# Kernel optimization log

Hardware: AMD Instinct MI355X
Metric: run time of the kernel (lower is better)

## Reference

```python
import jax, jax.numpy as jnp
import numpy as np

N = 100000        # nodes
E = 3200000       # edges (avg degree 32)
F_IN = 128        # input_dim
H = 64            # hidden_dim


def setup_inputs() -> dict:
    key = jax.random.key(0)
    ks = jax.random.split(key, 8)
    x = jax.random.normal(ks[0], (N, F_IN), dtype=jnp.float32)
    edge_index = jax.random.randint(ks[1], (2, E), 0, N, dtype=jnp.int64)
    # Glorot-ish init for GCNConv weights, zero bias (PyG default)
    def glorot(k, fan_in, fan_out):
        s = jnp.sqrt(6.0 / (fan_in + fan_out))
        return jax.random.uniform(k, (fan_in, fan_out), jnp.float32, -s, s)
    return {
        "x": x,
        "edge_index": edge_index,
        "W1": glorot(ks[2], F_IN, H), "b1": jnp.zeros((H,), jnp.float32),
        "W2": glorot(ks[3], H, H),    "b2": jnp.zeros((H,), jnp.float32),
        "W3": glorot(ks[4], H, H),    "b3": jnp.zeros((H,), jnp.float32),
    }


def _gcn_prep(edge_index):
    # add self-loops, compute symmetric normalization D^-1/2 (A+I) D^-1/2
    loop = jnp.arange(N, dtype=edge_index.dtype)
    src = jnp.concatenate([edge_index[0], loop])  # message sources
    dst = jnp.concatenate([edge_index[1], loop])  # aggregation targets
    deg = jax.ops.segment_sum(jnp.ones_like(dst, dtype=jnp.float32), dst, num_segments=N)
    dis = jnp.where(deg > 0, jax.lax.rsqrt(jnp.maximum(deg, 1.0)), 0.0)
    norm = dis[src] * dis[dst]  # [E+N]
    return src, dst, norm


def _gcn_conv(x, W, b, src, dst, norm):
    h = x @ W                                  # [N, H]
    msg = h[src] * norm[:, None]               # gather + scale, [E+N, H]
    out = jax.ops.segment_sum(msg, dst, num_segments=N)
    return out + b


def reference(x, edge_index, W1, b1, W2, b2, W3, b3):
    # GAEEncoder forward (eval mode: dropout p=0.2 is identity)
    src, dst, norm = _gcn_prep(edge_index)
    x = jax.nn.relu(_gcn_conv(x, W1, b1, src, dst, norm))
    x = jax.nn.relu(_gcn_conv(x, W2, b2, src, dst, norm))
    return _gcn_conv(x, W3, b3, src, dst, norm)
```

## Files before the change

kernel.cpp:

```cpp
#include <hip/hip_runtime.h>
#include <cstdint>

#define HDIM 64
#define BKT 98
#define BSHIFT 10
#define BCAP 36864

__device__ __forceinline__ float bflo(unsigned u) { return __uint_as_float(u << 16); }
__device__ __forceinline__ float bfhi(unsigned u) { return __uint_as_float(u & 0xffff0000u); }
__device__ __forceinline__ unsigned f2bf(float x) {
    unsigned b = __float_as_uint(x);
    return (b + 0x7fffu + ((b >> 16) & 1u)) >> 16;
}

__global__ void k_detect(const unsigned* ei, int* flag, int* tails) {
    __shared__ int ok;
    int t = threadIdx.x;
    if (t == 0) ok = 1;
    if (t < BKT) tails[t] = 0;
    __syncthreads();
    if (t < 128 && ei[2 * t + 1] != 0u) ok = 0;
    __syncthreads();
    if (t == 0) *flag = ok;
}

__device__ __forceinline__ int edge_val(const void* ei, int is64, long long idx) {
    if (is64) return (int)((const long long*)ei)[idx];
    return ((const int*)ei)[idx];
}

__global__ __launch_bounds__(1024) void k_bucket(const void* ei, const int* flag,
                                                 int* tails, unsigned* packed, int E) {
    __shared__ int wcnt[16][BKT];
    __shared__ int wbase[16][BKT];
    int tid = threadIdx.x;
    int lane = tid & 63, wid = tid >> 6;
    for (int i = tid; i < 16 * BKT; i += 1024) ((int*)wcnt)[i] = 0;
    __syncthreads();
    int is64 = *flag;
    int e = blockIdx.x * 1024 + tid;
    int b = -1; unsigned val = 0;
    if (e < E) {
        int d = edge_val(ei, is64, (long long)E + e);
        int s = edge_val(ei, is64, (long long)e);
        b = d >> BSHIFT;
        val = ((unsigned)(d & 1023) << 17) | (unsigned)s;
    }
    unsigned long long m = ~0ull;
#pragma unroll
    for (int bit = 0; bit < 7; bit++) {
        unsigned long long bb = __ballot(((unsigned)b >> bit) & 1);
        m &= ((((unsigned)b >> bit) & 1) ? bb : ~bb);
    }
    unsigned long long below = (lane == 0) ? 0ull : ((~0ull) >> (64 - lane));
    int rank = __popcll(m & below);
    if (b >= 0 && rank == 0) wcnt[wid][b] = __popcll(m);
    __syncthreads();
    if (tid < BKT) {
        int tot = 0;
        int pw[16];
#pragma unroll
        for (int w = 0; w < 16; w++) { pw[w] = tot; tot += wcnt[w][tid]; }
        int gb = (tot > 0) ? atomicAdd(&tails[tid], tot) : 0;
#pragma unroll
        for (int w = 0; w < 16; w++) wbase[w][tid] = gb + pw[w];
    }
    __syncthreads();
    if (b >= 0) {
        int pos = wbase[wid][b] + rank;
        if (pos < BCAP) packed[(size_t)b * BCAP + pos] = val;
    }
}

__global__ void k_base(const int* tails, int* bucket_base, int* rowptr, int N_) {
    __shared__ int sm[128];
    int t = threadIdx.x;
    int v = (t < BKT) ? min(tails[t], BCAP) : 0;
    sm[t] = v;
    __syncthreads();
    for (int off = 1; off < 128; off <<= 1) {
        int u = (t >= off) ? sm[t - off] : 0;
        __syncthreads();
        sm[t] += u;
        __syncthreads();
    }
    if (t < BKT) bucket_base[t] = sm[t] - v;
    if (t == BKT) { bucket_base[BKT] = sm[BKT - 1]; rowptr[N_] = sm[BKT - 1]; }
}

__global__ __launch_bounds__(1024) void k_build(const unsigned* packed, const int* tails,
                                                const int* bucket_base, int* rowptr,
                                                float* dis, int* col, int N_) {
    __shared__ int cnt[1024];
    __shared__ int pfx[1024];
    __shared__ int fill[1024];
    int b = blockIdx.x, tid = threadIdx.x;
    int nb_ = tails[b]; if (nb_ > BCAP) nb_ = BCAP;
    const unsigned* pb = packed + (size_t)b * BCAP;
    cnt[tid] = 0; fill[tid] = 0;
    __syncthreads();
    for (int s = tid; s < nb_; s += 1024)
        atomicAdd(&cnt[pb[s] >> 17], 1);
    __syncthreads();
    int v = cnt[tid];
    pfx[tid] = v;
    __syncthreads();
    for (int off = 1; off < 1024; off <<= 1) {
        int t = (tid >= off) ? pfx[tid - off] : 0;
        __syncthreads();
        pfx[tid] += t;
        __syncthreads();
    }
    int excl = pfx[tid] - v;
    int rowbase = bucket_base[b];
    int node = (b << BSHIFT) + tid;
    if (node < N_) {
        rowptr[node] = rowbase + excl;
        dis[node] = rsqrtf((float)(v + 1));
    }
    cnt[tid] = rowbase + excl;
    __syncthreads();
    for (int s = tid; s < nb_; s += 1024) {
        unsigned vv = pb[s];
        int dl = vv >> 17;
        int pos = cnt[dl] + atomicAdd(&fill[dl], 1);
        col[pos] = (int)(vv & 131071u);
    }
}

template <int K>
__device__ __forceinline__ int wswz(int lane, int k4) {
    if (K == 128) return k4 ^ (lane & 31);
    return ((k4 ^ (lane & 15)) + ((lane >> 4) << 2)) & 15;
}

template <int K, bool IN_BF16>
__global__ __launch_bounds__(256) void k_gemm_scale(const void* __restrict__ inp,
                                                    const float* __restrict__ W,
                                                    const float* __restrict__ dis,
                                                    unsigned* __restrict__ g2, int n) {
    constexpr int ROWS = (K == 128) ? 32 : 64;
    __shared__ float wt[64 * K];
    __shared__ float xs[ROWS * K];
    __shared__ float dsh[ROWS];
    int tid = threadIdx.x;
    for (int i = tid; i < K * 64; i += 256) {
        int k = i >> 6, f = i & 63;
        int k4 = k >> 2, j = k & 3;
        wt[f * K + (wswz<K>(f, k4) << 2) + j] = W[i];
    }
    int row0 = blockIdx.x * ROWS;
    int nrow = min(ROWS, n - row0);
    if (IN_BF16) {
        const unsigned* src = (const unsigned*)inp + (size_t)row0 * (K / 2);
        int nw = nrow * (K / 2);
        for (int i = tid; i < nw; i += 256) {
            unsigned u = src[i];
            xs[2 * i] = bflo(u);
            xs[2 * i + 1] = bfhi(u);
        }
    } else {
        const float4* src4 = (const float4*)((const float*)inp + (size_t)row0 * K);
        int nf4 = nrow * (K / 4);
        float4* xs4 = (float4*)xs;
        for (int i = tid; i < nf4; i += 256) xs4[i] = src4[i];
    }
    if (tid < nrow) dsh[tid] = dis[row0 + tid];
    __syncthreads();
    int lane = tid & 63, wid = tid >> 6;
    const float* wtl = wt + lane * K;
    constexpr int RW = ROWS / 4;
    for (int q = 0; q < RW; q += 4) {
        int rq = wid * RW + q;
        const float* x0 = xs + (size_t)(rq + 0) * K;
        const float* x1 = xs + (size_t)(rq + 1) * K;
        const float* x2 = xs + (size_t)(rq + 2) * K;
        const float* x3 = xs + (size_t)(rq + 3) * K;
        float a0 = 0.f, a1 = 0.f, a2 = 0.f, a3 = 0.f;
#pragma unroll 4
        for (int k4 = 0; k4 < K / 4; k4++) {
            float4 wv = *(const float4*)(wtl + (wswz<K>(lane, k4) << 2));
            float4 v0 = *(const float4*)(x0 + k4 * 4);
            float4 v1 = *(const float4*)(x1 + k4 * 4);
            float4 v2 = *(const float4*)(x2 + k4 * 4);
            float4 v3 = *(const float4*)(x3 + k4 * 4);
            a0 = fmaf(v0.x, wv.x, a0); a0 = fmaf(v0.y, wv.y, a0);
            a0 = fmaf(v0.z, wv.z, a0); a0 = fmaf(v0.w, wv.w, a0);
            a1 = fmaf(v1.x, wv.x, a1); a1 = fmaf(v1.y, wv.y, a1);
            a1 = fmaf(v1.z, wv.z, a1); a1 = fmaf(v1.w, wv.w, a1);
            a2 = fmaf(v2.x, wv.x, a2); a2 = fmaf(v2.y, wv.y, a2);
            a2 = fmaf(v2.z, wv.z, a2); a2 = fmaf(v2.w, wv.w, a2);
            a3 = fmaf(v3.x, wv.x, a3); a3 = fmaf(v3.y, wv.y, a3);
            a3 = fmaf(v3.z, wv.z, a3); a3 = fmaf(v3.w, wv.w, a3);
        }
        int gr = row0 + rq;
        bool wr = ((lane & 1) == 0);
        int wi = lane >> 1;
#pragma unroll
        for (int i = 0; i < 4; i++) {
            float a = (i == 0) ? a0 : (i == 1) ? a1 : (i == 2) ? a2 : a3;
            float v = a * dsh[rq + i];
            float p = __shfl_xor(v, 1);
            if (wr && gr + i < n)
                g2[(size_t)(gr + i) * 32 + wi] = f2bf(v) | (f2bf(p) << 16);
        }
    }
}

template <bool RELU, bool OUT32>
__global__ __launch_bounds__(256) void k_aggregate(const unsigned* __restrict__ g2,
                                                   const int* __restrict__ rowptr,
                                                   const int* __restrict__ col,
                                                   const float* __restrict__ dis,
                                                   const float* __restrict__ bias,
                                                   void* __restrict__ outp, int n) {
    int lane = threadIdx.x & 63;
    int wid = threadIdx.x >> 6;
    int li = lane & 15;
    int q = lane >> 4;
    int node = blockIdx.x * 4 + wid;
    if (node >= n) return;
    const uint2* g2v = (const uint2*)g2;
    float s0 = 0.f, s1 = 0.f, s2 = 0.f, s3 = 0.f;
    if (q == 0) {
        uint2 u = g2v[(size_t)node * 16 + li];
        s0 = bflo(u.x); s1 = bfhi(u.x); s2 = bflo(u.y); s3 = bfhi(u.y);
    }
    int e = rowptr[node], end = rowptr[node + 1];
    for (; e + 31 < end; e += 32) {
        int c0 = col[e + q],      c1 = col[e + 4 + q],  c2 = col[e + 8 + q],  c3 = col[e + 12 + q];
        int c4 = col[e + 16 + q], c5 = col[e + 20 + q], c6 = col[e + 24 + q], c7 = col[e + 28 + q];
        uint2 u0 = g2v[(size_t)c0 * 16 + li];
        uint2 u1 = g2v[(size_t)c1 * 16 + li];
        uint2 u2 = g2v[(size_t)c2 * 16 + li];
        uint2 u3 = g2v[(size_t)c3 * 16 + li];
        uint2 u4 = g2v[(size_t)c4 * 16 + li];
        uint2 u5 = g2v[(size_t)c5 * 16 + li];
        uint2 u6 = g2v[(size_t)c6 * 16 + li];
        uint2 u7 = g2v[(size_t)c7 * 16 + li];
        s0 += ((bflo(u0.x) + bflo(u1.x)) + (bflo(u2.x) + bflo(u3.x)))
            + ((bflo(u4.x) + bflo(u5.x)) + (bflo(u6.x) + bflo(u7.x)));
        s1 += ((bfhi(u0.x) + bfhi(u1.x)) + (bfhi(u2.x) + bfhi(u3.x)))
            + ((bfhi(u4.x) + bfhi(u5.x)) + (bfhi(u6.x) + bfhi(u7.x)));
        s2 += ((bflo(u0.y) + bflo(u1.y)) + (bflo(u2.y) + bflo(u3.y)))
            + ((bflo(u4.y) + bflo(u5.y)) + (bflo(u6.y) + bflo(u7.y)));
        s3 += ((bfhi(u0.y) + bfhi(u1.y)) + (bfhi(u2.y) + bfhi(u3.y)))
            + ((bfhi(u4.y) + bfhi(u5.y)) + (bfhi(u6.y) + bfhi(u7.y)));
    }
    for (; e + 15 < end; e += 16) {
        int c0 = col[e + q], c1 = col[e + 4 + q], c2 = col[e + 8 + q], c3 = col[e + 12 + q];
        uint2 u0 = g2v[(size_t)c0 * 16 + li];
        uint2 u1 = g2v[(size_t)c1 * 16 + li];
        uint2 u2 = g2v[(size_t)c2 * 16 + li];
        uint2 u3 = g2v[(size_t)c3 * 16 + li];
        s0 += ((bflo(u0.x) + bflo(u1.x)) + (bflo(u2.x) + bflo(u3.x)));
        s1 += ((bfhi(u0.x) + bfhi(u1.x)) + (bfhi(u2.x) + bfhi(u3.x)));
        s2 += ((bflo(u0.y) + bflo(u1.y)) + (bflo(u2.y) + bflo(u3.y)));
        s3 += ((bfhi(u0.y) + bfhi(u1.y)) + (bfhi(u2.y) + bfhi(u3.y)));
    }
    for (; e + 3 < end; e += 4) {
        int c = col[e + q];
        uint2 u = g2v[(size_t)c * 16 + li];
        s0 += bflo(u.x); s1 += bfhi(u.x); s2 += bflo(u.y); s3 += bfhi(u.y);
    }
    if (e < end) {
        int idx = e + q;
        bool valid = idx < end;
        int c = valid ? col[idx] : col[end - 1];
        uint2 u = g2v[(size_t)c * 16 + li];
        if (valid) { s0 += bflo(u.x); s1 += bfhi(u.x); s2 += bflo(u.y); s3 += bfhi(u.y); }
    }
    s0 += __shfl_xor(s0, 32); s0 += __shfl_xor(s0, 16);
    s1 += __shfl_xor(s1, 32); s1 += __shfl_xor(s1, 16);
    s2 += __shfl_xor(s2, 32); s2 += __shfl_xor(s2, 16);
    s3 += __shfl_xor(s3, 32); s3 += __shfl_xor(s3, 16);
    float4 b4 = ((const float4*)bias)[li];
    float dn = dis[node];
    float o0 = fmaf(dn, s0, b4.x);
    float o1 = fmaf(dn, s1, b4.y);
    float o2 = fmaf(dn, s2, b4.z);
    float o3 = fmaf(dn, s3, b4.w);
    if (RELU) {
        o0 = fmaxf(o0, 0.f); o1 = fmaxf(o1, 0.f);
        o2 = fmaxf(o2, 0.f); o3 = fmaxf(o3, 0.f);
    }
    if (q == 0) {
        if (OUT32) {
            ((float4*)outp)[(size_t)node * 16 + li] = make_float4(o0, o1, o2, o3);
        } else {
            uint2 st;
            st.x = f2bf(o0) | (f2bf(o1) << 16);
            st.y = f2bf(o2) | (f2bf(o3) << 16);
            ((uint2*)outp)[(size_t)node * 16 + li] = st;
        }
    }
}

extern "C" void kernel_launch(void* const* d_in, const int* in_sizes, int n_in,
                              void* d_out, int out_size, void* d_ws, size_t ws_size,
                              hipStream_t stream) {
    const float* x  = (const float*)d_in[0];
    const void*  ei = d_in[1];
    const float* W1 = (const float*)d_in[2];
    const float* b1 = (const float*)d_in[3];
    const float* W2 = (const float*)d_in[4];
    const float* b2 = (const float*)d_in[5];
    const float* W3 = (const float*)d_in[6];
    const float* b3 = (const float*)d_in[7];

    const int N = in_sizes[0] / 128;
    const int E = in_sizes[1] / 2;

    char* ws = (char*)d_ws;
    auto alloc = [&](size_t bytes) {
        char* p = ws;
        ws += ((bytes + 255) / 256) * 256;
        return p;
    };
    int*   flag   = (int*)alloc(4);
    int*   tails  = (int*)alloc(BKT * 4);
    int*   bbase  = (int*)alloc((BKT + 1) * 4);
    int*   rowptr = (int*)alloc((size_t)(N + 1) * 4);
    float* dis    = (float*)alloc((size_t)N * 4);
    int*   col    = (int*)alloc((size_t)E * 4);
    unsigned* bufA = (unsigned*)alloc((size_t)N * HDIM * 4);
    unsigned* bufB = (unsigned*)alloc((size_t)N * HDIM * 4);
    unsigned* packed = bufA;

    k_detect<<<1, 128, 0, stream>>>((const unsigned*)ei, flag, tails);
    k_bucket<<<(E + 1023) / 1024, 1024, 0, stream>>>(ei, flag, tails, packed, E);
    k_base<<<1, 128, 0, stream>>>(tails, bbase, rowptr, N);
    k_build<<<BKT, 1024, 0, stream>>>(packed, tails, bbase, rowptr, dis, col, N);

    const int aggGrid = (N + 3) / 4;

    k_gemm_scale<128, false><<<(N + 31) / 32, 256, 0, stream>>>(x, W1, dis, bufA, N);
    k_aggregate<true, false><<<aggGrid, 256, 0, stream>>>(bufA, rowptr, col, dis, b1, bufB, N);
    k_gemm_scale<64, true><<<(N + 63) / 64, 256, 0, stream>>>(bufB, W2, dis, bufA, N);
    k_aggregate<true, false><<<aggGrid, 256, 0, stream>>>(bufA, rowptr, col, dis, b2, bufB, N);
    k_gemm_scale<64, true><<<(N + 63) / 64, 256, 0, stream>>>(bufB, W3, dis, bufA, N);
    k_aggregate<false, true><<<aggGrid, 256, 0, stream>>>(bufA, rowptr, col, dis, b3, d_out, N);
}
```

Baseline: 445.6 us.

## Fold detect and base-scan kernels into bucket/build and coarsen bucket blocks

Removes the separate dtype-detect and bucket-prefix-scan kernels. Each bucket block now detects int64 itself, and each build block recomputes the 98-entry bucket prefix scan redundantly. The zeroing of tails moves to a memset. Each bucket block now processes 4096 edges instead of 1024, cutting the number of global atomicAdds on the tails array by about four times. The cost is more shared memory per bucket block and redundant small scans in every build block.

Measured after the change: 414.0 us, median of 2. 1.08x faster.

```diff
diff --git a/kernel.cpp b/kernel.cpp
--- a/kernel.cpp
+++ b/kernel.cpp
@@ -5,6 +5,7 @@
 #define BKT 98
 #define BSHIFT 10
 #define BCAP 36864
+#define ECHUNK 4096
 
 __device__ __forceinline__ float bflo(unsigned u) { return __uint_as_float(u << 16); }
 __device__ __forceinline__ float bfhi(unsigned u) { return __uint_as_float(u & 0xffff0000u); }
@@ -13,89 +14,91 @@
     return (b + 0x7fffu + ((b >> 16) & 1u)) >> 16;
 }
 
-__global__ void k_detect(const unsigned* ei, int* flag, int* tails) {
-    __shared__ int ok;
-    int t = threadIdx.x;
-    if (t == 0) ok = 1;
-    if (t < BKT) tails[t] = 0;
-    __syncthreads();
-    if (t < 128 && ei[2 * t + 1] != 0u) ok = 0;
-    __syncthreads();
-    if (t == 0) *flag = ok;
-}
-
 __device__ __forceinline__ int edge_val(const void* ei, int is64, long long idx) {
     if (is64) return (int)((const long long*)ei)[idx];
     return ((const int*)ei)[idx];
 }
 
-__global__ __launch_bounds__(1024) void k_bucket(const void* ei, const int* flag,
-                                                 int* tails, unsigned* packed, int E) {
-    __shared__ int wcnt[16][BKT];
-    __shared__ int wbase[16][BKT];
+__global__ __launch_bounds__(1024) void k_bucket(const unsigned* ei32, int* tails,
+                                                 unsigned* packed, int E) {
+    __shared__ int wcnt[4][16][BKT];
+    __shared__ int wpre[4][16][BKT];
+    __shared__ int gbase[BKT];
+    __shared__ int is64_s;
     int tid = threadIdx.x;
     int lane = tid & 63, wid = tid >> 6;
-    for (int i = tid; i < 16 * BKT; i += 1024) ((int*)wcnt)[i] = 0;
-    __syncthreads();
-    int is64 = *flag;
-    int e = blockIdx.x * 1024 + tid;
-    int b = -1; unsigned val = 0;
-    if (e < E) {
-        int d = edge_val(ei, is64, (long long)E + e);
-        int s = edge_val(ei, is64, (long long)e);
-        b = d >> BSHIFT;
-        val = ((unsigned)(d & 1023) << 17) | (unsigned)s;
-    }
-    unsigned long long m = ~0ull;
-#pragma unroll
-    for (int bit = 0; bit < 7; bit++) {
-        unsigned long long bb = __ballot(((unsigned)b >> bit) & 1);
-        m &= ((((unsigned)b >> bit) & 1) ? bb : ~bb);
-    }
+    for (int i = tid; i < 4 * 16 * BKT; i += 1024) ((int*)wcnt)[i] = 0;
+    if (tid == 0) is64_s = 1;
+    __syncthreads();
+    if (tid < 128 && ei32[2 * tid + 1] != 0u) is64_s = 0;
+    __syncthreads();
+    int is64 = is64_s;
+    const void* ei = ei32;
+    int b[4]; unsigned val[4]; int rank[4];
+    int e0 = blockIdx.x * ECHUNK;
     unsigned long long below = (lane == 0) ? 0ull : ((~0ull) >> (64 - lane));
-    int rank = __popcll(m & below);
-    if (b >= 0 && rank == 0) wcnt[wid][b] = __popcll(m);
+#pragma unroll
+    for (int r = 0; r < 4; r++) {
+        int e = e0 + r * 1024 + tid;
+        b[r] = -1; val[r] = 0;
+        if (e < E) {
+            int d = edge_val(ei, is64, (long long)E + e);
+            int s = edge_val(ei, is64, (long long)e);
+            b[r] = d >> BSHIFT;
+            val[r] = ((unsigned)(d & 1023) << 17) | (unsigned)s;
+        }
+        unsigned long long m = ~0ull;
+#pragma unroll
+        for (int bit = 0; bit < 7; bit++) {
+            unsigned long long bb = __ballot(((unsigned)b[r] >> bit) & 1);
+            m &= ((((unsigned)b[r] >> bit) & 1) ? bb : ~bb);
+        }
+        rank[r] = __popcll(m & below);
+        if (b[r] >= 0 && rank[r] == 0) wcnt[r][wid][b[r]] = __popcll(m);
+    }
     __syncthreads();
     if (tid < BKT) {
         int tot = 0;
-        int pw[16];
-#pragma unroll
-        for (int w = 0; w < 16; w++) { pw[w] = tot; tot += wcnt[w][tid]; }
-        int gb = (tot > 0) ? atomicAdd(&tails[tid], tot) : 0;
-#pragma unroll
-        for (int w = 0; w < 16; w++) wbase[w][tid] = gb + pw[w];
-    }
-    __syncthreads();
-    if (b >= 0) {
-        int pos = wbase[wid][b] + rank;
-        if (pos < BCAP) packed[(size_t)b * BCAP + pos] = val;
-    }
-}
-
-__global__ void k_base(const int* tails, int* bucket_base, int* rowptr, int N_) {
-    __shared__ int sm[128];
-    int t = threadIdx.x;
-    int v = (t < BKT) ? min(tails[t], BCAP) : 0;
-    sm[t] = v;
-    __syncthreads();
-    for (int off = 1; off < 128; off <<= 1) {
-        int u = (t >= off) ? sm[t - off] : 0;
-        __syncthreads();
-        sm[t] += u;
-        __syncthreads();
-    }
-    if (t < BKT) bucket_base[t] = sm[t] - v;
-    if (t == BKT) { bucket_base[BKT] = sm[BKT - 1]; rowptr[N_] = sm[BKT - 1]; }
+#pragma unroll
+        for (int r = 0; r < 4; r++)
+#pragma unroll
+            for (int w = 0; w < 16; w++) {
+                wpre[r][w][tid] = tot;
+                tot += wcnt[r][w][tid];
+            }
+        gbase[tid] = (tot > 0) ? atomicAdd(&tails[tid], tot) : 0;
+    }
+    __syncthreads();
+#pragma unroll
+    for (int r = 0; r < 4; r++) {
+        if (b[r] >= 0) {
+            int pos = gbase[b[r]] + wpre[r][wid][b[r]] + rank[r];
+            if (pos < BCAP) packed[(size_t)b[r] * BCAP + pos] = val[r];
+        }
+    }
 }
 
 __global__ __launch_bounds__(1024) void k_build(const unsigned* packed, const int* tails,
-                                                const int* bucket_base, int* rowptr,
-                                                float* dis, int* col, int N_) {
+                                                int* rowptr, float* dis, int* col, int N_) {
     __shared__ int cnt[1024];
     __shared__ int pfx[1024];
     __shared__ int fill[1024];
+    __shared__ int rb_s;
     int b = blockIdx.x, tid = threadIdx.x;
-    int nb_ = tails[b]; if (nb_ > BCAP) nb_ = BCAP;
+    int v0 = (tid < BKT) ? min(tails[tid], BCAP) : 0;
+    if (tid < 128) pfx[tid] = v0;
+    __syncthreads();
+    for (int off = 1; off < 128; off <<= 1) {
+        int u = (tid >= off && tid < 128) ? pfx[tid - off] : 0;
+        __syncthreads();
+        if (tid < 128) pfx[tid] += u;
+        __syncthreads();
+    }
+    if (tid == b) rb_s = pfx[tid] - v0;
+    if (b == 0 && tid == BKT - 1) rowptr[N_] = pfx[BKT - 1];
+    __syncthreads();
+    int rowbase = rb_s;
+    int nb_ = min(tails[b], BCAP);
     const unsigned* pb = packed + (size_t)b * BCAP;
     cnt[tid] = 0; fill[tid] = 0;
     __syncthreads();
@@ -112,7 +115,6 @@
         __syncthreads();
     }
     int excl = pfx[tid] - v;
-    int rowbase = bucket_base[b];
     int node = (b << BSHIFT) + tid;
     if (node < N_) {
         rowptr[node] = rowbase + excl;
@@ -317,9 +319,7 @@
         ws += ((bytes + 255) / 256) * 256;
         return p;
     };
-    int*   flag   = (int*)alloc(4);
     int*   tails  = (int*)alloc(BKT * 4);
-    int*   bbase  = (int*)alloc((BKT + 1) * 4);
     int*   rowptr = (int*)alloc((size_t)(N + 1) * 4);
     float* dis    = (float*)alloc((size_t)N * 4);
     int*   col    = (int*)alloc((size_t)E * 4);
@@ -327,10 +327,9 @@
     unsigned* bufB = (unsigned*)alloc((size_t)N * HDIM * 4);
     unsigned* packed = bufA;
 
-    k_detect<<<1, 128, 0, stream>>>((const unsigned*)ei, flag, tails);
-    k_bucket<<<(E + 1023) / 1024, 1024, 0, stream>>>(ei, flag, tails, packed, E);
-    k_base<<<1, 128, 0, stream>>>(tails, bbase, rowptr, N);
-    k_build<<<BKT, 1024, 0, stream>>>(packed, tails, bbase, rowptr, dis, col, N);
+    hipMemsetAsync(tails, 0, BKT * 4, stream);
+    k_bucket<<<(E + ECHUNK - 1) / ECHUNK, 1024, 0, stream>>>((const unsigned*)ei, tails, packed, E);
+    k_build<<<BKT, 1024, 0, stream>>>(packed, tails, rowptr, dis, col, N);
 
     const int aggGrid = (N + 3) / 4;
 
```
